# Kernel tuning notes

Measured on AMD Instinct MI355X. Metric: run time of the kernel, lower is better.

## Reference

```python
import jax, jax.numpy as jnp
import numpy as np

N_NODES = 50000
N_EDGES = 800000
HIDDEN = 128
IN_DIM = 128
OUT_DIM = 40
N_LAYERS = 3


def setup_inputs() -> dict:
    key = jax.random.key(0)
    ks = jax.random.split(key, 8)
    s = 1.0 / np.sqrt(HIDDEN)
    return {
        "x": jax.random.normal(ks[0], (N_NODES, IN_DIM), jnp.float32),
        "edge_index": jax.random.randint(ks[1], (2, N_EDGES), 0, N_NODES, jnp.int32),
        "W_in": jax.random.normal(ks[2], (IN_DIM, HIDDEN), jnp.float32) * s,
        "b_in": jnp.zeros((HIDDEN,), jnp.float32),
        "Wl": jax.random.normal(ks[3], (N_LAYERS, HIDDEN, HIDDEN), jnp.float32) * s,
        "Wr": jax.random.normal(ks[4], (N_LAYERS, HIDDEN, HIDDEN), jnp.float32) * s,
        "bl": jnp.zeros((N_LAYERS, HIDDEN), jnp.float32),
        "Wc1": jax.random.normal(ks[5], (HIDDEN, HIDDEN), jnp.float32) * s,
        "bc1": jnp.zeros((HIDDEN,), jnp.float32),
        "Wc2": jax.random.normal(ks[6], (HIDDEN, OUT_DIM), jnp.float32) * s,
        "bc2": jnp.zeros((OUT_DIM,), jnp.float32),
    }


def reference(x, edge_index, W_in, b_in, Wl, Wr, bl, Wc1, bc1, Wc2, bc2):
    src, dst = edge_index[0], edge_index[1]
    n = x.shape[0]
    # in-degree for mean aggregation (clamped to 1 for isolated nodes)
    deg = jax.ops.segment_sum(jnp.ones_like(src, x.dtype), dst, num_segments=n)
    deg_inv = (1.0 / jnp.maximum(deg, 1.0))[:, None]  # [N,1]

    h = x @ W_in + b_in  # lin1; dropout is identity in eval mode
    js = []
    for i in range(N_LAYERS):
        # GraphSAGE-mean: gather neighbor feats, scatter-mean, self + neighbor linear
        agg = jax.ops.segment_sum(h[src], dst, num_segments=n) * deg_inv
        h = jax.nn.relu(h @ Wl[i] + agg @ Wr[i] + bl[i])
        js.append(h)  # skip ops are identity; fix_last appends last layer directly

    x5 = js[0] + js[1] + js[2]  # layer aggregator 'l_sum' with linear activation
    hc = jax.nn.relu(x5 @ Wc1 + bc1)
    return hc @ Wc2 + bc2  # logits [N, OUT_DIM]
```

## Files before the change

### kernel.cpp

```cpp
#include <hip/hip_runtime.h>

#define NN   50000
#define NE   800000
#define HID  128
#define OUTD 40
#define NBLK 196

typedef float f32x4  __attribute__((ext_vector_type(4)));
typedef int   i32x4  __attribute__((ext_vector_type(4)));
typedef short bf16x8 __attribute__((ext_vector_type(8)));

__device__ __forceinline__ f32x4 mfma(bf16x8 a, bf16x8 b, f32x4 c) {
  return __builtin_amdgcn_mfma_f32_16x16x32_bf16(a, b, c, 0, 0, 0);
}
__device__ __forceinline__ unsigned short f2bf(float f) {
  unsigned u = __builtin_bit_cast(unsigned, f);
  u += 0x7fffu + ((u >> 16) & 1u);
  return (unsigned short)(u >> 16);
}
__device__ __forceinline__ unsigned pack2(float lo, float hi) {
  return (unsigned)f2bf(lo) | ((unsigned)f2bf(hi) << 16);
}
__device__ __forceinline__ float bflo(unsigned v){ return __builtin_bit_cast(float, v << 16); }
__device__ __forceinline__ float bfhi(unsigned v){ return __builtin_bit_cast(float, v & 0xffff0000u); }

__global__ void k_deg(const int* __restrict__ dst, int* __restrict__ deg,
                      int* __restrict__ pos) {
  int i = blockIdx.x * blockDim.x + threadIdx.x;
  if (i < NE) pos[i] = atomicAdd(&deg[dst[i]], 1);
}

__global__ void k_blocksum(const int* __restrict__ deg, int* __restrict__ bsum) {
  __shared__ int s[256];
  int t = threadIdx.x, i = blockIdx.x * 256 + t;
  s[t] = (i < NN) ? deg[i] : 0;
  __syncthreads();
  for (int o = 128; o > 0; o >>= 1) { if (t < o) s[t] += s[t + o]; __syncthreads(); }
  if (t == 0) bsum[blockIdx.x] = s[0];
}

__global__ void k_scan3(const int* __restrict__ deg, const int* __restrict__ bsum,
                        int* __restrict__ offs, float* __restrict__ dinv) {
  __shared__ int sb[256];
  __shared__ int s[256];
  int t = threadIdx.x, i = blockIdx.x * 256 + t;
  sb[t] = (t < NBLK && t < blockIdx.x) ? bsum[t] : 0;
  int v = (i < NN) ? deg[i] : 0;
  s[t] = v;
  __syncthreads();
  for (int o = 128; o > 0; o >>= 1) { if (t < o) sb[t] += sb[t + o]; __syncthreads(); }
  for (int o = 1; o < 256; o <<= 1) {
    int x = (t >= o) ? s[t - o] : 0;
    __syncthreads(); s[t] += x; __syncthreads();
  }
  int off = sb[0] + s[t] - v;
  if (i < NN) {
    offs[i] = off;
    dinv[i] = 1.0f / (float)(v > 0 ? v : 1);
  }
  if (i == 0) offs[NN] = NE;
}

__global__ void k_fill(const int* __restrict__ src, const int* __restrict__ dst,
                       const int* __restrict__ pos, const int* __restrict__ offs,
                       int* __restrict__ csr) {
  int i = blockIdx.x * blockDim.x + threadIdx.x;
  if (i < NE) {
    csr[offs[dst[i]] + pos[i]] = src[i];
  }
}

__global__ void k_prep(const float* __restrict__ Win, const float* __restrict__ Wl,
                       const float* __restrict__ Wr, const float* __restrict__ Wc1,
                       const float* __restrict__ Wc2, unsigned short* __restrict__ wt,
                       int* __restrict__ deg) {
  int idx = blockIdx.x * 256 + threadIdx.x;
  if (idx < NN) deg[idx] = 0;
  const int NMAIN = 8 * 16384;
  if (idx >= NMAIN + 48 * 128) return;
  float v;
  if (idx < NMAIN) {
    int m = idx >> 14, rem = idx & 16383;
    int n = rem >> 7, k = rem & 127;
    const float* s;
    if (m == 0) s = Win;
    else if (m <= 3) s = Wl + (m - 1) * 16384;
    else if (m <= 6) s = Wr + (m - 4) * 16384;
    else s = Wc1;
    v = s[k * 128 + n];
  } else {
    int rem = idx - NMAIN;
    int n = rem >> 7, k = rem & 127;
    v = (n < OUTD) ? Wc2[k * OUTD + n] : 0.f;
  }
  wt[idx] = f2bf(v);
}

__global__ __launch_bounds__(256) void k_agg(const unsigned short* __restrict__ h,
                                             const int* __restrict__ csr,
                                             const int* __restrict__ offs,
                                             const float* __restrict__ dinv,
                                             unsigned short* __restrict__ agg) {
  const int lane = threadIdx.x & 63;
  const int l31 = lane & 31;
  const int hi = lane >> 5;
  int gw = (blockIdx.x * blockDim.x + threadIdx.x) >> 6;
  int nw = (gridDim.x * blockDim.x) >> 6;
  const uint2* h2 = (const uint2*)h;
  uint2* ag2 = (uint2*)agg;
  for (int n = gw; n < NN; n += nw) {
    int s = offs[n], e = offs[n + 1];
    float a0 = 0, a1 = 0, a2 = 0, a3 = 0;
    float b0 = 0, b1 = 0, b2 = 0, b3 = 0;
    float c0 = 0, c1 = 0, c2 = 0, c3 = 0;
    float d0 = 0, d1 = 0, d2 = 0, d3 = 0;
    int k = s;
    int r0, r1, r2, r3;
    bool have = (k + 8 <= e);
    if (have) {
      r0 = csr[k + 0 + hi]; r1 = csr[k + 2 + hi];
      r2 = csr[k + 4 + hi]; r3 = csr[k + 6 + hi];
    }
    while (have) {
      uint2 v0 = h2[r0 * 32 + l31];
      uint2 v1 = h2[r1 * 32 + l31];
      uint2 v2 = h2[r2 * 32 + l31];
      uint2 v3 = h2[r3 * 32 + l31];
      k += 8;
      have = (k + 8 <= e);
      if (have) {
        r0 = csr[k + 0 + hi]; r1 = csr[k + 2 + hi];
        r2 = csr[k + 4 + hi]; r3 = csr[k + 6 + hi];
      }
      a0 += bflo(v0.x); a1 += bfhi(v0.x); a2 += bflo(v0.y); a3 += bfhi(v0.y);
      b0 += bflo(v1.x); b1 += bfhi(v1.x); b2 += bflo(v1.y); b3 += bfhi(v1.y);
      c0 += bflo(v2.x); c1 += bfhi(v2.x); c2 += bflo(v2.y); c3 += bfhi(v2.y);
      d0 += bflo(v3.x); d1 += bfhi(v3.x); d2 += bflo(v3.y); d3 += bfhi(v3.y);
    }
    for (; k + 2 <= e; k += 2) {
      int r = csr[k + hi];
      uint2 v = h2[r * 32 + l31];
      a0 += bflo(v.x); a1 += bfhi(v.x); a2 += bflo(v.y); a3 += bfhi(v.y);
    }
    if (k < e) {
      int r = csr[k];
      uint2 v = h2[r * 32 + l31];
      if (hi == 0) {
        a0 += bflo(v.x); a1 += bfhi(v.x); a2 += bflo(v.y); a3 += bfhi(v.y);
      }
    }
    float s0 = a0 + b0 + c0 + d0, s1 = a1 + b1 + c1 + d1;
    float s2 = a2 + b2 + c2 + d2, s3 = a3 + b3 + c3 + d3;
    s0 += __shfl_xor(s0, 32); s1 += __shfl_xor(s1, 32);
    s2 += __shfl_xor(s2, 32); s3 += __shfl_xor(s3, 32);
    float di = dinv[n];
    if (hi == 0) {
      uint2 o;
      o.x = pack2(s0 * di, s1 * di);
      o.y = pack2(s2 * di, s3 * di);
      ag2[n * 32 + l31] = o;
    }
  }
}

__global__ __launch_bounds__(256) void k_lin_in(const float* __restrict__ x,
                                                const unsigned short* __restrict__ Wt,
                                                const float* __restrict__ bias,
                                                unsigned short* __restrict__ hout) {
  const int lane = threadIdx.x & 63, w = threadIdx.x >> 6;
  const int wr = w >> 1, wc = w & 1;
  const int r15 = lane & 15, khi = lane >> 4;
  const int mbase = blockIdx.x * 128 + wr * 64, nbase = wc * 64;
  f32x4 acc[4][4] = {};
#pragma unroll
  for (int ks = 0; ks < 4; ++ks) {
    const int kk = ks * 32 + khi * 8;
    bf16x8 af[4], bq[4];
#pragma unroll
    for (int i = 0; i < 4; i++) {
      int row = mbase + i * 16 + r15; row = row < NN ? row : NN - 1;
      const f32x4* p = (const f32x4*)(x + row * HID + kk);
      f32x4 lo = p[0], hi = p[1];
      i32x4 t;
      t[0] = pack2(lo[0], lo[1]); t[1] = pack2(lo[2], lo[3]);
      t[2] = pack2(hi[0], hi[1]); t[3] = pack2(hi[2], hi[3]);
      af[i] = __builtin_bit_cast(bf16x8, t);
    }
#pragma unroll
    for (int j = 0; j < 4; j++) {
      int col = nbase + j * 16 + r15;
      bq[j] = *(const bf16x8*)(Wt + col * HID + kk);
    }
#pragma unroll
    for (int i = 0; i < 4; i++)
#pragma unroll
      for (int j = 0; j < 4; j++) acc[i][j] = mfma(af[i], bq[j], acc[i][j]);
  }
  float b4[4];
#pragma unroll
  for (int j = 0; j < 4; j++) b4[j] = bias[nbase + j * 16 + r15];
#pragma unroll
  for (int i = 0; i < 4; i++) {
    const int rb = mbase + i * 16 + khi * 4;
#pragma unroll
    for (int e = 0; e < 4; e++) {
      const int r = rb + e;
      if (r < NN) {
#pragma unroll
        for (int j = 0; j < 4; j++)
          hout[r * HID + nbase + j * 16 + r15] = f2bf(acc[i][j][e] + b4[j]);
      }
    }
  }
}

__global__ __launch_bounds__(256) void k_layer(const unsigned short* __restrict__ hp,
                                               const unsigned short* __restrict__ ag,
                                               const unsigned short* __restrict__ WtL,
                                               const unsigned short* __restrict__ WtR,
                                               const float* __restrict__ bias,
                                               unsigned short* __restrict__ hout) {
  const int lane = threadIdx.x & 63, w = threadIdx.x >> 6;
  const int wr = w >> 1, wc = w & 1;
  const int r15 = lane & 15, khi = lane >> 4;
  const int mbase = blockIdx.x * 128 + wr * 64, nbase = wc * 64;
  f32x4 acc[4][4] = {};
#pragma unroll
  for (int ph = 0; ph < 2; ++ph) {
    const unsigned short* A = ph ? ag : hp;
    const unsigned short* B = ph ? WtR : WtL;
#pragma unroll
    for (int ks = 0; ks < 4; ++ks) {
      const int kk = ks * 32 + khi * 8;
      bf16x8 af[4], bq[4];
#pragma unroll
      for (int i = 0; i < 4; i++) {
        int row = mbase + i * 16 + r15; row = row < NN ? row : NN - 1;
        af[i] = *(const bf16x8*)(A + row * HID + kk);
      }
#pragma unroll
      for (int j = 0; j < 4; j++) {
        int col = nbase + j * 16 + r15;
        bq[j] = *(const bf16x8*)(B + col * HID + kk);
      }
#pragma unroll
      for (int i = 0; i < 4; i++)
#pragma unroll
        for (int j = 0; j < 4; j++) acc[i][j] = mfma(af[i], bq[j], acc[i][j]);
    }
  }
  float b4[4];
#pragma unroll
  for (int j = 0; j < 4; j++) b4[j] = bias[nbase + j * 16 + r15];
#pragma unroll
  for (int i = 0; i < 4; i++) {
    const int rb = mbase + i * 16 + khi * 4;
#pragma unroll
    for (int e = 0; e < 4; e++) {
      const int r = rb + e;
      if (r < NN) {
#pragma unroll
        for (int j = 0; j < 4; j++) {
          float v = acc[i][j][e] + b4[j];
          v = fmaxf(v, 0.f);
          hout[r * HID + nbase + j * 16 + r15] = f2bf(v);
        }
      }
    }
  }
}

__global__ __launch_bounds__(256) void k_cls(const unsigned short* __restrict__ h1,
                                             const unsigned short* __restrict__ h2,
                                             const unsigned short* __restrict__ h3,
                                             const unsigned short* __restrict__ WtC1,
                                             const float* __restrict__ bc1,
                                             const unsigned short* __restrict__ WtC2,
                                             const float* __restrict__ bc2,
                                             float* __restrict__ out) {
  __shared__ unsigned short hc[128 * 136];
  const int lane = threadIdx.x & 63, w = threadIdx.x >> 6;
  const int wr = w >> 1, wc = w & 1;
  const int r15 = lane & 15, khi = lane >> 4;
  const int mbase = blockIdx.x * 128 + wr * 64, nbase = wc * 64;
  {
    f32x4 acc[4][4] = {};
#pragma unroll
    for (int ks = 0; ks < 4; ++ks) {
      const int kk = ks * 32 + khi * 8;
      bf16x8 af[4], bq[4];
#pragma unroll
      for (int i = 0; i < 4; i++) {
        int row = mbase + i * 16 + r15; row = row < NN ? row : NN - 1;
        i32x4 u = *(const i32x4*)(h1 + row * HID + kk);
        i32x4 v = *(const i32x4*)(h2 + row * HID + kk);
        i32x4 q = *(const i32x4*)(h3 + row * HID + kk);
        i32x4 t;
#pragma unroll
        for (int c = 0; c < 4; c++) {
          unsigned uu = u[c], vv = v[c], qq = q[c];
          t[c] = pack2(bflo(uu) + bflo(vv) + bflo(qq), bfhi(uu) + bfhi(vv) + bfhi(qq));
        }
        af[i] = __builtin_bit_cast(bf16x8, t);
      }
#pragma unroll
      for (int j = 0; j < 4; j++) {
        int col = nbase + j * 16 + r15;
        bq[j] = *(const bf16x8*)(WtC1 + col * HID + kk);
      }
#pragma unroll
      for (int i = 0; i < 4; i++)
#pragma unroll
        for (int j = 0; j < 4; j++) acc[i][j] = mfma(af[i], bq[j], acc[i][j]);
    }
    float b4[4];
#pragma unroll
    for (int j = 0; j < 4; j++) b4[j] = bc1[nbase + j * 16 + r15];
#pragma unroll
    for (int i = 0; i < 4; i++) {
      const int rT = wr * 64 + i * 16 + khi * 4;
#pragma unroll
      for (int e = 0; e < 4; e++) {
#pragma unroll
        for (int j = 0; j < 4; j++) {
          float v = fmaxf(acc[i][j][e] + b4[j], 0.f);
          hc[(rT + e) * 136 + nbase + j * 16 + r15] = f2bf(v);
        }
      }
    }
  }
  __syncthreads();
  {
    f32x4 a2[2][3] = {};
#pragma unroll
    for (int ks = 0; ks < 4; ++ks) {
      const int kk = ks * 32 + khi * 8;
      bf16x8 af[2], bq[3];
#pragma unroll
      for (int i = 0; i < 2; i++) {
        int rT = w * 32 + i * 16 + r15;
        af[i] = *(const bf16x8*)&hc[rT * 136 + kk];
      }
#pragma unroll
      for (int j = 0; j < 3; j++) {
        int col = j * 16 + r15;
        bq[j] = *(const bf16x8*)(WtC2 + col * HID + kk);
      }
#pragma unroll
      for (int i = 0; i < 2; i++)
#pragma unroll
        for (int j = 0; j < 3; j++) a2[i][j] = mfma(af[i], bq[j], a2[i][j]);
    }
#pragma unroll
    for (int j = 0; j < 3; j++) {
      const int col = j * 16 + r15;
      const float b = (col < OUTD) ? bc2[col] : 0.f;
#pragma unroll
      for (int i = 0; i < 2; i++) {
        const int rT = w * 32 + i * 16 + khi * 4;
#pragma unroll
        for (int e = 0; e < 4; e++) {
          const int gr = blockIdx.x * 128 + rT + e;
          if (gr < NN && col < OUTD) out[gr * OUTD + col] = a2[i][j][e] + b;
        }
      }
    }
  }
}

extern "C" void kernel_launch(void* const* d_in, const int* in_sizes, int n_in,
                              void* d_out, int out_size, void* d_ws, size_t ws_size,
                              hipStream_t stream) {
  (void)in_sizes; (void)n_in; (void)out_size; (void)ws_size;
  const float* x   = (const float*)d_in[0];
  const int*   ei  = (const int*)d_in[1];
  const float* Win = (const float*)d_in[2];
  const float* bin = (const float*)d_in[3];
  const float* Wl  = (const float*)d_in[4];
  const float* Wr  = (const float*)d_in[5];
  const float* bl  = (const float*)d_in[6];
  const float* Wc1 = (const float*)d_in[7];
  const float* bc1 = (const float*)d_in[8];
  const float* Wc2 = (const float*)d_in[9];
  const float* bc2 = (const float*)d_in[10];
  float* out = (float*)d_out;

  char* ws = (char*)d_ws;
  size_t off = 0;
  auto take = [&](size_t bytes) -> char* {
    char* p = ws + off; off = (off + bytes + 255) & ~(size_t)255; return p;
  };
  int* deg        = (int*)take((size_t)NN * 4);
  int* offs       = (int*)take((size_t)(NN + 1) * 4);
  int* pos        = (int*)take((size_t)NE * 4);
  int* bsum       = (int*)take(256 * 4);
  float* dinv     = (float*)take((size_t)NN * 4);
  int* csr        = (int*)take((size_t)NE * 4);
  unsigned short* wt  = (unsigned short*)take((size_t)(8 * 16384 + 48 * 128) * 2);
  unsigned short* h0  = (unsigned short*)take((size_t)NN * HID * 2);
  unsigned short* h1  = (unsigned short*)take((size_t)NN * HID * 2);
  unsigned short* h2  = (unsigned short*)take((size_t)NN * HID * 2);
  unsigned short* h3  = (unsigned short*)take((size_t)NN * HID * 2);
  unsigned short* agg = (unsigned short*)take((size_t)NN * HID * 2);

  const int* esrc = ei;
  const int* edst = ei + NE;

  k_prep<<<(8 * 16384 + 48 * 128 + 255) / 256, 256, 0, stream>>>(Win, Wl, Wr, Wc1, Wc2, wt, deg);
  k_deg<<<(NE + 255) / 256, 256, 0, stream>>>(edst, deg, pos);
  k_blocksum<<<NBLK, 256, 0, stream>>>(deg, bsum);
  k_scan3<<<NBLK, 256, 0, stream>>>(deg, bsum, offs, dinv);
  k_fill<<<(NE + 255) / 256, 256, 0, stream>>>(esrc, edst, pos, offs, csr);
  k_lin_in<<<(NN + 127) / 128, 256, 0, stream>>>(x, wt, bin, h0);

  unsigned short* hs[4] = {h0, h1, h2, h3};
  for (int i = 0; i < 3; i++) {
    k_agg<<<2048, 256, 0, stream>>>(hs[i], csr, offs, dinv, agg);
    k_layer<<<(NN + 127) / 128, 256, 0, stream>>>(hs[i], agg, wt + (1 + i) * 16384,
                                                  wt + (4 + i) * 16384, bl + i * HID, hs[i + 1]);
  }
  k_cls<<<(NN + 127) / 128, 256, 0, stream>>>(h1, h2, h3, wt + 7 * 16384, bc1,
                                              wt + 8 * 16384, bc2, out);
}
```

Baseline: 255.0 us.

## Store hidden features column-sliced so aggregation gathers fit in cache

Hidden activations are stored in four column slices of 32 features each, laid out [slice][node][32], instead of row-major. The aggregation kernel launches four passes, one grid quarter per slice, so each pass gathers from a 3.2 MB slice that can stay resident in cache. Each wavefront reads 64-byte rows for four neighbors at once and reduces the partial sums with shuffles. The GEMM kernels read and write through the new address mapping. The cost is more CSR index reads, since the edge list is walked once per slice, and narrower 64-byte gather segments.

```diff
diff --git a/kernel.cpp b/kernel.cpp
--- a/kernel.cpp
+++ b/kernel.cpp
@@ -23,6 +23,10 @@
 }
 __device__ __forceinline__ float bflo(unsigned v){ return __builtin_bit_cast(float, v << 16); }
 __device__ __forceinline__ float bfhi(unsigned v){ return __builtin_bit_cast(float, v & 0xffff0000u); }
+
+__device__ __forceinline__ int haddr(int row, int col) {
+  return (col >> 5) * (NN * 32) + row * 32 + (col & 31);
+}
 
 __global__ void k_deg(const int* __restrict__ dst, int* __restrict__ deg,
                       int* __restrict__ pos) {
@@ -102,63 +106,43 @@
                                              const float* __restrict__ dinv,
                                              unsigned short* __restrict__ agg) {
   const int lane = threadIdx.x & 63;
-  const int l31 = lane & 31;
-  const int hi = lane >> 5;
-  int gw = (blockIdx.x * blockDim.x + threadIdx.x) >> 6;
-  int nw = (gridDim.x * blockDim.x) >> 6;
-  const uint2* h2 = (const uint2*)h;
-  uint2* ag2 = (uint2*)agg;
+  const int c = lane & 15;
+  const int q = lane >> 4;
+  const int pass = blockIdx.x >> 11;
+  const int bid = blockIdx.x & 2047;
+  int gw = (bid * 256 + (int)threadIdx.x) >> 6;
+  const int nw = 2048 * 4;
+  const unsigned* hs = (const unsigned*)(h + (size_t)pass * (NN * 32));
+  unsigned* ag32 = (unsigned*)agg;
   for (int n = gw; n < NN; n += nw) {
-    int s = offs[n], e = offs[n + 1];
-    float a0 = 0, a1 = 0, a2 = 0, a3 = 0;
-    float b0 = 0, b1 = 0, b2 = 0, b3 = 0;
-    float c0 = 0, c1 = 0, c2 = 0, c3 = 0;
-    float d0 = 0, d1 = 0, d2 = 0, d3 = 0;
+    const int s = offs[n], e = offs[n + 1];
+    float f0=0,f1=0,f2=0,f3=0,f4=0,f5=0,f6=0,f7=0;
     int k = s;
-    int r0, r1, r2, r3;
-    bool have = (k + 8 <= e);
-    if (have) {
-      r0 = csr[k + 0 + hi]; r1 = csr[k + 2 + hi];
-      r2 = csr[k + 4 + hi]; r3 = csr[k + 6 + hi];
-    }
+    int i0, i1, i2, i3;
+    bool have = (k + 16 <= e);
+    if (have) { i0=csr[k+q]; i1=csr[k+4+q]; i2=csr[k+8+q]; i3=csr[k+12+q]; }
     while (have) {
-      uint2 v0 = h2[r0 * 32 + l31];
-      uint2 v1 = h2[r1 * 32 + l31];
-      uint2 v2 = h2[r2 * 32 + l31];
-      uint2 v3 = h2[r3 * 32 + l31];
-      k += 8;
-      have = (k + 8 <= e);
-      if (have) {
-        r0 = csr[k + 0 + hi]; r1 = csr[k + 2 + hi];
-        r2 = csr[k + 4 + hi]; r3 = csr[k + 6 + hi];
-      }
-      a0 += bflo(v0.x); a1 += bfhi(v0.x); a2 += bflo(v0.y); a3 += bfhi(v0.y);
-      b0 += bflo(v1.x); b1 += bfhi(v1.x); b2 += bflo(v1.y); b3 += bfhi(v1.y);
-      c0 += bflo(v2.x); c1 += bfhi(v2.x); c2 += bflo(v2.y); c3 += bfhi(v2.y);
-      d0 += bflo(v3.x); d1 += bfhi(v3.x); d2 += bflo(v3.y); d3 += bfhi(v3.y);
-    }
-    for (; k + 2 <= e; k += 2) {
-      int r = csr[k + hi];
-      uint2 v = h2[r * 32 + l31];
-      a0 += bflo(v.x); a1 += bfhi(v.x); a2 += bflo(v.y); a3 += bfhi(v.y);
-    }
-    if (k < e) {
-      int r = csr[k];
-      uint2 v = h2[r * 32 + l31];
-      if (hi == 0) {
-        a0 += bflo(v.x); a1 += bfhi(v.x); a2 += bflo(v.y); a3 += bfhi(v.y);
-      }
-    }
-    float s0 = a0 + b0 + c0 + d0, s1 = a1 + b1 + c1 + d1;
-    float s2 = a2 + b2 + c2 + d2, s3 = a3 + b3 + c3 + d3;
-    s0 += __shfl_xor(s0, 32); s1 += __shfl_xor(s1, 32);
-    s2 += __shfl_xor(s2, 32); s3 += __shfl_xor(s3, 32);
-    float di = dinv[n];
-    if (hi == 0) {
-      uint2 o;
-      o.x = pack2(s0 * di, s1 * di);
-      o.y = pack2(s2 * di, s3 * di);
-      ag2[n * 32 + l31] = o;
+      unsigned u0 = hs[i0*16+c], u1 = hs[i1*16+c], u2 = hs[i2*16+c], u3 = hs[i3*16+c];
+      k += 16;
+      have = (k + 16 <= e);
+      if (have) { i0=csr[k+q]; i1=csr[k+4+q]; i2=csr[k+8+q]; i3=csr[k+12+q]; }
+      f0 += bflo(u0); f1 += bfhi(u0);
+      f2 += bflo(u1); f3 += bfhi(u1);
+      f4 += bflo(u2); f5 += bfhi(u2);
+      f6 += bflo(u3); f7 += bfhi(u3);
+    }
+    for (; k < e; k += 4) {
+      if (k + q < e) {
+        unsigned u = hs[csr[k + q] * 16 + c];
+        f0 += bflo(u); f1 += bfhi(u);
+      }
+    }
+    float slo = (f0 + f2) + (f4 + f6), shi = (f1 + f3) + (f5 + f7);
+    slo += __shfl_xor(slo, 16); shi += __shfl_xor(shi, 16);
+    slo += __shfl_xor(slo, 32); shi += __shfl_xor(shi, 32);
+    if (q == 0) {
+      float di = dinv[n];
+      ag32[n * 64 + pass * 16 + c] = pack2(slo * di, shi * di);
     }
   }
 }
@@ -208,7 +192,7 @@
       if (r < NN) {
 #pragma unroll
         for (int j = 0; j < 4; j++)
-          hout[r * HID + nbase + j * 16 + r15] = f2bf(acc[i][j][e] + b4[j]);
+          hout[haddr(r, nbase + j * 16 + r15)] = f2bf(acc[i][j][e] + b4[j]);
       }
     }
   }
@@ -236,7 +220,7 @@
 #pragma unroll
       for (int i = 0; i < 4; i++) {
         int row = mbase + i * 16 + r15; row = row < NN ? row : NN - 1;
-        af[i] = *(const bf16x8*)(A + row * HID + kk);
+        af[i] = *(const bf16x8*)(A + (ph ? (row * HID + kk) : haddr(row, kk)));
       }
 #pragma unroll
       for (int j = 0; j < 4; j++) {
@@ -263,7 +247,7 @@
         for (int j = 0; j < 4; j++) {
           float v = acc[i][j][e] + b4[j];
           v = fmaxf(v, 0.f);
-          hout[r * HID + nbase + j * 16 + r15] = f2bf(v);
+          hout[haddr(r, nbase + j * 16 + r15)] = f2bf(v);
         }
       }
     }
@@ -292,14 +276,15 @@
 #pragma unroll
       for (int i = 0; i < 4; i++) {
         int row = mbase + i * 16 + r15; row = row < NN ? row : NN - 1;
-        i32x4 u = *(const i32x4*)(h1 + row * HID + kk);
-        i32x4 v = *(const i32x4*)(h2 + row * HID + kk);
-        i32x4 q = *(const i32x4*)(h3 + row * HID + kk);
+        const int ha = haddr(row, kk);
+        i32x4 u = *(const i32x4*)(h1 + ha);
+        i32x4 v = *(const i32x4*)(h2 + ha);
+        i32x4 q = *(const i32x4*)(h3 + ha);
         i32x4 t;
 #pragma unroll
-        for (int c = 0; c < 4; c++) {
-          unsigned uu = u[c], vv = v[c], qq = q[c];
-          t[c] = pack2(bflo(uu) + bflo(vv) + bflo(qq), bfhi(uu) + bfhi(vv) + bfhi(qq));
+        for (int cc = 0; cc < 4; cc++) {
+          unsigned uu = u[cc], vv = v[cc], qq = q[cc];
+          t[cc] = pack2(bflo(uu) + bflo(vv) + bflo(qq), bfhi(uu) + bfhi(vv) + bfhi(qq));
         }
         af[i] = __builtin_bit_cast(bf16x8, t);
       }
@@ -415,7 +400,7 @@
 
   unsigned short* hs[4] = {h0, h1, h2, h3};
   for (int i = 0; i < 3; i++) {
-    k_agg<<<2048, 256, 0, stream>>>(hs[i], csr, offs, dinv, agg);
+    k_agg<<<8192, 256, 0, stream>>>(hs[i], csr, offs, dinv, agg);
     k_layer<<<(NN + 127) / 128, 256, 0, stream>>>(hs[i], agg, wt + (1 + i) * 16384,
                                                   wt + (4 + i) * 16384, bl + i * HID, hs[i + 1]);
   }
```

Result: slower. 376.3 us (+47.6%).
